# Kernel optimization log

Measured on AMD Instinct MI355X. Metric: run time of the kernel, lower is better.

Reference implementation:

```python
import jax, jax.numpy as jnp
import numpy as np
import math

NUM_CLASSES = 80
MAX_ANCHOR_MATCHES = 10
ALPHA = 0.5
BETA = 6.0
EPSILON = 1e-9        # label-encoder epsilon
KEPS = 1e-7           # keras.backend.epsilon() used inside compute_ciou
B, NB = 16, 64        # batch, padded max GT boxes


def make_anchor_points():
    # YOLOv8 @ 640x640: strides 8/16/32 -> 80^2 + 40^2 + 20^2 = 8400 anchors
    pts = []
    for stride, n in [(8, 80), (16, 40), (32, 20)]:
        xs = (jnp.arange(n, dtype=jnp.float32) + 0.5) * stride
        gy, gx = jnp.meshgrid(xs, xs, indexing='ij')
        pts.append(jnp.stack([gx.reshape(-1), gy.reshape(-1)], axis=-1))
    return jnp.concatenate(pts, axis=0)  # (8400, 2)


def setup_inputs() -> dict:
    key = jax.random.key(0)
    k0, k1, k2, k3, k4, k5 = jax.random.split(key, 6)
    anc_points = make_anchor_points()
    NA = anc_points.shape[0]
    pd_scores = jax.random.uniform(k0, (B, NA, NUM_CLASSES), dtype=jnp.float32)
    # predicted boxes roughly centered on anchors
    wh = jax.random.uniform(k1, (B, NA, 2), minval=8.0, maxval=96.0)
    ctr = anc_points[None] + jax.random.normal(k2, (B, NA, 2)) * 8.0
    pd_bboxes = jnp.concatenate([ctr - wh / 2, ctr + wh / 2], axis=-1)
    # ground-truth boxes (xyxy) inside a 640x640 image
    g_wh = jax.random.uniform(k3, (B, NB, 2), minval=16.0, maxval=200.0)
    g_ctr = jax.random.uniform(k4, (B, NB, 2), minval=40.0, maxval=600.0)
    gt_bboxes = jnp.concatenate([g_ctr - g_wh / 2, g_ctr + g_wh / 2], axis=-1)
    gt_labels = jax.random.randint(k5, (B, NB), 0, NUM_CLASSES).astype(jnp.float32)
    # first 48 of 64 padded slots are real boxes
    mask_gt = jnp.broadcast_to(jnp.arange(NB)[None, :, None] < 48, (B, NB, 1))
    return {
        'pd_scores': pd_scores,
        'pd_bboxes': pd_bboxes,
        'anc_points': anc_points,
        'gt_labels': gt_labels,
        'gt_bboxes': gt_bboxes,
        'mask_gt': mask_gt,
    }


def compute_ciou(b1, b2):
    """CIoU between xyxy boxes b1 (gt) and b2 (pred); broadcasts, returns (...,)."""
    x1a, y1a, x2a, y2a = b1[..., 0], b1[..., 1], b1[..., 2], b1[..., 3]
    x1b, y1b, x2b, y2b = b2[..., 0], b2[..., 1], b2[..., 2], b2[..., 3]
    w1 = x2a - x1a
    h1 = y2a - y1a + KEPS
    w2 = x2b - x1b
    h2 = y2b - y1b + KEPS
    inter = (jnp.maximum(jnp.minimum(x2a, x2b) - jnp.maximum(x1a, x1b), 0.0)
             * jnp.maximum(jnp.minimum(y2a, y2b) - jnp.maximum(y1a, y1b), 0.0))
    union = w1 * h1 + w2 * h2 - inter + KEPS
    iou = inter / union
    cw = jnp.maximum(x2a, x2b) - jnp.minimum(x1a, x1b)
    ch = jnp.maximum(y2a, y2b) - jnp.minimum(y1a, y1b)
    c2 = cw * cw + ch * ch + KEPS
    rho2 = ((x1a + x2a) / 2 - (x1b + x2b) / 2) ** 2 + ((y1a + y2a) / 2 - (y1b + y2b) / 2) ** 2
    v = (4.0 / math.pi ** 2) * (jnp.arctan(w2 / h2) - jnp.arctan(w1 / h1)) ** 2
    alpha = v / (v - iou + (1.0 + KEPS))
    return iou - (rho2 / c2 + v * alpha)


def _encode(pd_scores, pd_bboxes, anc_points, gt_labels, gt_bboxes, mask_gt):
    Bn, NA, NC = pd_scores.shape
    NBn = gt_bboxes.shape[1]
    f32 = pd_scores.dtype
    mask_gt_b = mask_gt.astype(bool)                      # (B, NB, 1)

    # --- select_candidates_in_gts: anchor center inside gt box ---
    lt = gt_bboxes[:, :, None, :2]                        # (B, NB, 1, 2)
    rb = gt_bboxes[:, :, None, 2:]
    anc = anc_points[None, None, :, :]                    # (1, 1, NA, 2)
    deltas = jnp.concatenate([anc - lt, rb - anc], -1)    # (B, NB, NA, 4)
    mask_in_gts = jnp.min(deltas, axis=-1) > EPSILON      # (B, NB, NA)
    valid = mask_in_gts & mask_gt_b                       # (B, NB, NA)

    # --- get_box_metrics ---
    lbl = jnp.maximum(gt_labels.astype(jnp.int32), 0)     # (B, NB)
    sc = jnp.take_along_axis(pd_scores, jnp.broadcast_to(lbl[:, None, :], (Bn, NA, NBn)), axis=-1)
    sc = jnp.transpose(sc, (0, 2, 1))                     # (B, NB, NA)
    sc = jnp.where(gt_labels[:, :, None] >= 0, sc, 0.0)
    bbox_scores = jnp.where(valid, sc, 0.0)
    iou = compute_ciou(gt_bboxes[:, :, None, :], pd_bboxes[:, None, :, :])  # (B, NB, NA)
    iou = jnp.where(iou > 0, iou, 0.0)
    overlaps = jnp.where(valid, iou, 0.0)
    align_metric = jnp.power(bbox_scores, ALPHA) * jnp.power(overlaps, BETA)

    # --- select_topk_candidates ---
    k = MAX_ANCHOR_MATCHES
    _, topk_idxs = jax.lax.top_k(align_metric, k)         # (B, NB, k)
    topk_idxs = jnp.where(jnp.broadcast_to(mask_gt_b, (Bn, NBn, k)), topk_idxs, 0)
    bi = jnp.arange(Bn)[:, None, None]
    gi = jnp.arange(NBn)[None, :, None]
    counts = jnp.zeros((Bn, NBn, NA), f32).at[bi, gi, topk_idxs].add(1.0)
    mask_topk = jnp.where(counts > 1, 0.0, counts)        # drop idx-0 duplicates
    mask_pos = mask_topk * mask_in_gts.astype(f32) * mask_gt_b.astype(f32)

    # --- select_highest_overlaps (tie-break anchors matched to >1 gt) ---
    fg_mask = jnp.sum(mask_pos, axis=-2)                  # (B, NA)
    mask_multi = jnp.broadcast_to((fg_mask > 1)[:, None, :], (Bn, NBn, NA))
    max_idx = jnp.argmax(overlaps, axis=1)                # (B, NA)
    is_max = jnp.transpose(jax.nn.one_hot(max_idx, NBn, dtype=f32), (0, 2, 1))
    mask_pos = jnp.where(mask_multi, is_max, mask_pos)
    fg_mask = jnp.sum(mask_pos, axis=-2)
    target_gt_idx = jnp.argmax(mask_pos, axis=-2)         # (B, NA)

    # --- get_targets ---
    target_labels = jnp.take_along_axis(lbl, target_gt_idx, axis=1)          # (B, NA)
    target_bboxes = jnp.take_along_axis(gt_bboxes, target_gt_idx[..., None], axis=1)  # (B, NA, 4)
    target_scores = jax.nn.one_hot(target_labels, NC, dtype=f32)
    target_scores = jnp.where((fg_mask > 0)[..., None], target_scores, 0.0)

    # --- normalize class targets by alignment metric ---
    align_metric = align_metric * mask_pos
    pos_align = jnp.max(align_metric, axis=-1, keepdims=True)                # (B, NB, 1)
    pos_overlaps = jnp.max(overlaps * mask_pos, axis=-1, keepdims=True)
    norm = jnp.max(align_metric * pos_overlaps / (pos_align + EPSILON), axis=-2)[..., None]
    target_scores = target_scores * norm
    return target_bboxes, target_scores, fg_mask


def reference(pd_scores, pd_bboxes, anc_points, gt_labels, gt_bboxes, mask_gt):
    tb, ts, fg = _encode(pd_scores, pd_bboxes, anc_points, gt_labels, gt_bboxes, mask_gt)
    return (jax.lax.stop_gradient(tb), jax.lax.stop_gradient(ts), jax.lax.stop_gradient(fg))
```

## Files before the change

kernel.cpp:

```cpp
#include <hip/hip_runtime.h>
#include <cstdint>
#include <cstddef>

#define NBg 64
#define NCg 80
#define KTOP 10
#define K16 16

typedef unsigned long long u64k;

__device__ __forceinline__ float ciou_dev(float gx1, float gy1, float gx2, float gy2,
                                          float px1, float py1, float px2, float py2) {
#pragma clang fp contract(off)
  const float keps = 1e-7f;
  float w1 = gx2 - gx1;
  float h1 = (gy2 - gy1) + keps;
  float w2 = px2 - px1;
  float h2 = (py2 - py1) + keps;
  float iw = fminf(gx2, px2) - fmaxf(gx1, px1);
  float ih = fminf(gy2, py2) - fmaxf(gy1, py1);
  float inter = fmaxf(iw, 0.0f) * fmaxf(ih, 0.0f);
  float uni = w1 * h1 + w2 * h2 - inter + keps;
  float iou = inter / uni;
  float cw = fmaxf(gx2, px2) - fminf(gx1, px1);
  float ch = fmaxf(gy2, py2) - fminf(gy1, py1);
  float c2 = cw * cw + ch * ch + keps;
  float dx = (gx1 + gx2) * 0.5f - (px1 + px2) * 0.5f;
  float dy = (gy1 + gy2) * 0.5f - (py1 + py2) * 0.5f;
  float rho2 = dx * dx + dy * dy;
  float q2 = w2 / h2;
  float q1 = w1 / h1;
  float t = (float)atan((double)q2) - (float)atan((double)q1);
  float v = 0.4052847345693511f * (t * t);
  float alpha = v / ((v - iou) + 1.0000001f);
  return iou - (rho2 / c2 + v * alpha);
}

__device__ __forceinline__ float am_dev(float sc, float ov) {
  float f1 = (float)sqrt((double)sc);
  double o = (double)ov;
  double o3 = o * o * o;
  return f1 * (float)(o3 * o3);
}

__device__ __forceinline__ u64k mk_key(float am, int a) {
  return ((u64k)__float_as_uint(am) << 32) | (unsigned)(~a);
}

__device__ __forceinline__ void merge16(u64k (&L)[K16], const u64k (&B)[K16]) {
  u64k C[K16];
#pragma unroll
  for (int i = 0; i < K16; i++) {
    u64k x = L[i], y = B[15 - i];
    C[i] = x > y ? x : y;
  }
#pragma unroll
  for (int s = 8; s > 0; s >>= 1) {
#pragma unroll
    for (int i = 0; i < K16; i++) {
      if ((i & s) == 0) {
        u64k x = C[i], y = C[i | s];
        C[i] = x > y ? x : y;
        C[i | s] = x > y ? y : x;
      }
    }
  }
#pragma unroll
  for (int i = 0; i < K16; i++) L[i] = C[i];
}

__global__ void ka_topk(const float* __restrict__ pd_scores,
                        const float* __restrict__ pd_bboxes,
                        const float* __restrict__ anc,
                        const float* __restrict__ gt_labels,
                        const float* __restrict__ gt_bboxes,
                        const int* __restrict__ mask_gt,
                        int* __restrict__ sel,
                        float* __restrict__ posAlign,
                        float* __restrict__ posOv,
                        int NA) {
  int row = blockIdx.x;
  int tid = threadIdx.x;
  int lane = tid & 63;
  int wid = tid >> 6;
  if (tid == 0) { posAlign[row] = 0.0f; posOv[row] = 0.0f; }
  if (!mask_gt[row]) {
    if (tid < KTOP) sel[row * KTOP + tid] = -1;
    return;
  }
  int b = row >> 6;
  const float* g = gt_bboxes + (size_t)row * 4;
  float gx1 = g[0], gy1 = g[1], gx2 = g[2], gy2 = g[3];
  float gl = gt_labels[row];
  int lbl = gl > 0.0f ? (int)gl : 0;
  bool glpos = (gl >= 0.0f);

  auto rect = [&](float s, int n, int& x0, int& y0, int& w, int& h) {
    int i0 = (int)floorf(gx1 / s - 0.5f) - 1; if (i0 < 0) i0 = 0;
    int i1 = (int)ceilf (gx2 / s - 0.5f) + 1; if (i1 > n - 1) i1 = n - 1;
    int j0 = (int)floorf(gy1 / s - 0.5f) - 1; if (j0 < 0) j0 = 0;
    int j1 = (int)ceilf (gy2 / s - 0.5f) + 1; if (j1 > n - 1) j1 = n - 1;
    x0 = i0; y0 = j0;
    w = i1 - i0 + 1; h = j1 - j0 + 1;
    if (w < 0) w = 0;
    if (h < 0) h = 0;
  };
  int x00, y00, w0, h0, x01, y01, w1, h1, x02, y02, w2, h2;
  rect( 8.0f, 80, x00, y00, w0, h0);
  rect(16.0f, 40, x01, y01, w1, h1);
  rect(32.0f, 20, x02, y02, w2, h2);
  int sz0 = w0 * h0, sz1 = w1 * h1, sz2 = w2 * h2;
  int tot = sz0 + sz1 + sz2;

  u64k k[KTOP];
#pragma unroll
  for (int q = 0; q < KTOP; q++) k[q] = 0;

  auto ins = [&](u64k key) {
    if (key > k[KTOP - 1]) {
      k[KTOP - 1] = key;
#pragma unroll
      for (int q = KTOP - 1; q > 0; q--) {
        if (k[q] > k[q - 1]) { u64k t = k[q]; k[q] = k[q - 1]; k[q - 1] = t; }
      }
    }
  };

  for (int c = tid; c < tot; c += 256) {
    int cc, x0, y0, w, nbase, ngrid; float ss;
    if (c < sz0)              { cc = c;              x0 = x00; y0 = y00; w = w0; nbase = 0;    ngrid = 80; ss =  8.0f; }
    else if (c < sz0 + sz1)   { cc = c - sz0;        x0 = x01; y0 = y01; w = w1; nbase = 6400; ngrid = 40; ss = 16.0f; }
    else                      { cc = c - sz0 - sz1;  x0 = x02; y0 = y02; w = w2; nbase = 8000; ngrid = 20; ss = 32.0f; }
    int iy = y0 + cc / w;
    int ix = x0 + cc % w;
    float ax = ((float)ix + 0.5f) * ss;
    float ay = ((float)iy + 0.5f) * ss;
    float dmin = fminf(fminf(ax - gx1, ay - gy1), fminf(gx2 - ax, gy2 - ay));
    if (dmin > 1e-9f) {
      int a = nbase + iy * ngrid + ix;
      const float4 pb = ((const float4*)pd_bboxes)[(size_t)b * NA + a];
      float ci = ciou_dev(gx1, gy1, gx2, gy2, pb.x, pb.y, pb.z, pb.w);
      float ov = ci > 0.0f ? ci : 0.0f;
      float sc = glpos ? pd_scores[((size_t)b * NA + a) * NCg + lbl] : 0.0f;
      ins(mk_key(am_dev(sc, ov), a));
    }
  }

  u64k L[K16];
#pragma unroll
  for (int q = 0; q < KTOP; q++) L[q] = k[q];
#pragma unroll
  for (int q = KTOP; q < K16; q++) L[q] = 0;

#pragma unroll
  for (int step = 0; step < 6; step++) {
    u64k B[K16];
#pragma unroll
    for (int q = 0; q < K16; q++)
      B[q] = __shfl_xor((unsigned long long)L[q], 1 << step, 64);
    merge16(L, B);
  }

  __shared__ u64k xl[4][K16];
  if (lane < K16) xl[wid][lane] = L[lane];
  __syncthreads();
  if (wid == 2) {
    u64k B[K16];
#pragma unroll
    for (int q = 0; q < K16; q++) B[q] = xl[3][q];
    merge16(L, B);
    if (lane < K16) xl[2][lane] = L[lane];
  }
  if (wid == 0) {
    u64k B[K16];
#pragma unroll
    for (int q = 0; q < K16; q++) B[q] = xl[1][q];
    merge16(L, B);
  }
  __syncthreads();
  if (wid == 0) {
    u64k B[K16];
#pragma unroll
    for (int q = 0; q < K16; q++) B[q] = xl[2][q];
    merge16(L, B);
    if (lane == 0) {
      int npos = 0;
#pragma unroll
      for (int q = 0; q < KTOP; q++) if ((L[q] >> 32) != 0) npos++;
      int cand = 0;
      const float2* anc2 = (const float2*)anc;
      for (int slot = 0; slot < KTOP; slot++) {
        int a;
        if (slot < npos) {
          a = (int)~(unsigned)L[slot];
        } else {
          bool moved = true;
          while (moved) {
            moved = false;
#pragma unroll
            for (int q = 0; q < KTOP; q++)
              if (q < npos && (int)~(unsigned)L[q] == cand) { cand++; moved = true; }
          }
          a = cand++;
        }
        float2 ap = anc2[a];
        float dmin = fminf(fminf(ap.x - gx1, ap.y - gy1),
                           fminf(gx2 - ap.x, gy2 - ap.y));
        sel[row * KTOP + slot] = (dmin > 1e-9f) ? a : -1;
      }
    }
  }
}

__global__ void k3_resolve(const float* __restrict__ pd_scores,
                           const float* __restrict__ pd_bboxes,
                           const float* __restrict__ anc,
                           const float* __restrict__ gt_labels,
                           const float* __restrict__ gt_bboxes,
                           const int* __restrict__ mask_gt,
                           const int* __restrict__ sel,
                           int* __restrict__ tgt,
                           float* __restrict__ amv,
                           float* __restrict__ out_tb,
                           float* __restrict__ out_fg,
                           float* __restrict__ posAlign,
                           float* __restrict__ posOv,
                           int NA) {
  int b = blockIdx.y;
  int tid = threadIdx.x;
  int a0 = blockIdx.x * 256;
  int a = a0 + tid;
  __shared__ float4 sg[NBg];
  __shared__ int svalid[NBg];
  __shared__ int slbl[NBg];
  __shared__ int sglpos[NBg];
  __shared__ unsigned int mlo[256];
  __shared__ unsigned int mhi[256];
  mlo[tid] = 0u; mhi[tid] = 0u;
  if (tid < NBg) {
    int j = tid;
    const float* g = gt_bboxes + ((size_t)b * NBg + j) * 4;
    sg[j] = make_float4(g[0], g[1], g[2], g[3]);
    svalid[j] = mask_gt[b * NBg + j];
    float gl = gt_labels[b * NBg + j];
    slbl[j] = gl > 0.0f ? (int)gl : 0;
    sglpos[j] = (gl >= 0.0f) ? 1 : 0;
  }
  __syncthreads();
  for (int i = tid; i < NBg * KTOP; i += 256) {
    int e = sel[b * NBg * KTOP + i];
    int d = e - a0;
    if (d >= 0 && d < 256) {
      int j = i / KTOP;
      unsigned int bit = 1u << (j & 31);
      if (j < 32) atomicOr(&mlo[d], bit); else atomicOr(&mhi[d], bit);
    }
  }
  __syncthreads();
  if (a >= NA) return;
  unsigned int lo = mlo[tid], hi = mhi[tid];
  int cnt = __popc(lo) + __popc(hi);
  int first = lo ? (__ffs(lo) - 1) : (hi ? 32 + __ffs(hi) - 1 : 0);

  float ax = anc[2 * a], ay = anc[2 * a + 1];
  float px1 = 0.f, py1 = 0.f, px2 = 0.f, py2 = 0.f;
  if (cnt > 0) {
    const float* pb = pd_bboxes + ((size_t)b * NA + a) * 4;
    px1 = pb[0]; py1 = pb[1]; px2 = pb[2]; py2 = pb[3];
  }
  int t = 0;
  float fg = 0.0f;
  float ovt = -1.0f;
  if (cnt == 1) {
    t = first; fg = 1.0f;
  } else if (cnt > 1) {
    unsigned bm_lo = 0u, bm_hi = 0u;
    for (int jj = 0; jj < NBg; jj++) {
      if (svalid[jj]) {
        float4 gq = sg[jj];
        float dmin = fminf(fminf(ax - gq.x, ay - gq.y), fminf(gq.z - ax, gq.w - ay));
        if (dmin > 1e-9f) {
          if (jj < 32) bm_lo |= 1u << jj; else bm_hi |= 1u << (jj - 32);
        }
      }
    }
    float best = 0.0f;
    t = 0;
    unsigned m = bm_lo; int base = 0;
    for (int half = 0; half < 2; half++) {
      while (m) {
        int jj = base + __ffs(m) - 1; m &= m - 1;
        float4 gq = sg[jj];
        float ci = ciou_dev(gq.x, gq.y, gq.z, gq.w, px1, py1, px2, py2);
        float ov = ci > 0.0f ? ci : 0.0f;
        if (ov > best) { best = ov; t = jj; }
      }
      m = bm_hi; base = 32;
    }
    fg = 1.0f;
    ovt = best;
  }
  tgt[(size_t)b * NA + a] = t;
  out_fg[(size_t)b * NA + a] = fg;
  float4 gb = sg[t];
  ((float4*)out_tb)[(size_t)b * NA + a] = gb;
  float amval = 0.0f;
  if (fg > 0.0f) {
    float ov;
    if (ovt >= 0.0f) {
      ov = ovt;
    } else {
      float ci = ciou_dev(gb.x, gb.y, gb.z, gb.w, px1, py1, px2, py2);
      ov = ci > 0.0f ? ci : 0.0f;
    }
    float sc = sglpos[t] ? pd_scores[((size_t)b * NA + a) * NCg + slbl[t]] : 0.0f;
    amval = am_dev(sc, ov);
    atomicMax((int*)(posAlign + b * NBg + t), __float_as_int(amval));
    atomicMax((int*)(posOv + b * NBg + t), __float_as_int(ov));
  }
  amv[(size_t)b * NA + a] = amval;
}

__global__ void k5_scores(const float* __restrict__ gt_labels,
                          const int* __restrict__ tgt,
                          const float* __restrict__ out_fg,
                          const float* __restrict__ amv,
                          const float* __restrict__ posAlign,
                          const float* __restrict__ posOv,
                          float* __restrict__ out_ts,
                          int NA) {
  int b = blockIdx.y;
  int a0 = blockIdx.x * 256;
  int tid = threadIdx.x;
  int a = a0 + tid;
  __shared__ float snorm[256];
  __shared__ int slab[256];
  float norm = 0.0f;
  int lbl = -1;
  if (a < NA) {
    int t = tgt[(size_t)b * NA + a];
    float fg = out_fg[(size_t)b * NA + a];
    if (fg > 0.0f) {
      float av = amv[(size_t)b * NA + a];
      norm = av * posOv[b * NBg + t] / (posAlign[b * NBg + t] + 1e-9f);
      float gl = gt_labels[b * NBg + t];
      lbl = gl > 0.0f ? (int)gl : 0;
    }
  }
  snorm[tid] = norm;
  slab[tid] = lbl;
  __syncthreads();
  int nanch = NA - a0; if (nanch > 256) nanch = 256;
  int nf4 = nanch * (NCg / 4);
  float4* o = (float4*)(out_ts + ((size_t)b * NA + a0) * NCg);
  for (int i = tid; i < nf4; i += 256) {
    int aa = i / (NCg / 4);
    int c0 = (i % (NCg / 4)) * 4;
    int lb = slab[aa];
    float nv = snorm[aa];
    float4 w = make_float4(0.0f, 0.0f, 0.0f, 0.0f);
    int d = lb - c0;
    if (d >= 0 && d < 4) ((float*)&w)[d] = nv;
    o[i] = w;
  }
}

extern "C" void kernel_launch(void* const* d_in, const int* in_sizes, int n_in,
                              void* d_out, int out_size, void* d_ws, size_t ws_size,
                              hipStream_t stream) {
  const float* pd_scores = (const float*)d_in[0];
  const float* pd_bboxes = (const float*)d_in[1];
  const float* anc       = (const float*)d_in[2];
  const float* gt_labels = (const float*)d_in[3];
  const float* gt_bboxes = (const float*)d_in[4];
  const int*   mask_gt   = (const int*)d_in[5];

  int NA = in_sizes[2] / 2;
  int B  = in_sizes[3] / NBg;
  size_t nBA = (size_t)B * NA;

  float* out_tb = (float*)d_out;
  float* out_ts = out_tb + nBA * 4;
  float* out_fg = out_ts + nBA * NCg;

  char* ws = (char*)d_ws;
  size_t off = 0;
  int* sel = (int*)(ws + off);                off += (size_t)B * NBg * KTOP * 4;
  int* tgt = (int*)(ws + off);                off += nBA * 4;
  float* amv = (float*)(ws + off);            off += nBA * 4;
  float* posAlign = (float*)(ws + off);       off += (size_t)B * NBg * 4;
  float* posOv = (float*)(ws + off);          off += (size_t)B * NBg * 4;

  dim3 blk(256);
  int rows = B * NBg;
  ka_topk<<<rows, blk, 0, stream>>>(pd_scores, pd_bboxes, anc, gt_labels,
                                    gt_bboxes, mask_gt, sel, posAlign, posOv, NA);
  dim3 gA((NA + 255) / 256, B);
  k3_resolve<<<gA, blk, 0, stream>>>(pd_scores, pd_bboxes, anc, gt_labels,
                                     gt_bboxes, mask_gt, sel, tgt, amv,
                                     out_tb, out_fg, posAlign, posOv, NA);
  k5_scores<<<gA, blk, 0, stream>>>(gt_labels, tgt, out_fg, amv, posAlign, posOv,
                                    out_ts, NA);
}
```

Measured before the change: 158.4 us.

## Fuse top-k, resolve and score kernels into one persistent kernel with grid barriers

Merges the three kernels into a single launch of 512 blocks that sync through a software grid barrier. Each block handles two GT rows for top-k selection, using 128 threads per row, and then up to two anchor tiles for the resolve and score phases. Per-anchor target and alignment values now stay in shared memory, so the tgt/amv workspace round trips and two kernel launches are removed. It adds a memset launch and depends on every block being co-resident; if they are not, the spin barrier can deadlock.

After: 324.2 us. 2.05x slower.

```diff
diff --git a/kernel.cpp b/kernel.cpp
--- a/kernel.cpp
+++ b/kernel.cpp
@@ -69,88 +69,131 @@
   for (int i = 0; i < K16; i++) L[i] = C[i];
 }
 
-__global__ void ka_topk(const float* __restrict__ pd_scores,
-                        const float* __restrict__ pd_bboxes,
-                        const float* __restrict__ anc,
-                        const float* __restrict__ gt_labels,
-                        const float* __restrict__ gt_bboxes,
-                        const int* __restrict__ mask_gt,
-                        int* __restrict__ sel,
-                        float* __restrict__ posAlign,
-                        float* __restrict__ posOv,
-                        int NA) {
-  int row = blockIdx.x;
+__device__ __forceinline__ void grid_barrier(unsigned* cnt, unsigned* gen) {
+  __syncthreads();
+  if (threadIdx.x == 0) {
+    __threadfence();
+    unsigned g = __hip_atomic_load(gen, __ATOMIC_RELAXED, __HIP_MEMORY_SCOPE_AGENT);
+    unsigned arrived =
+        __hip_atomic_fetch_add(cnt, 1u, __ATOMIC_ACQ_REL, __HIP_MEMORY_SCOPE_AGENT) + 1;
+    if (arrived == gridDim.x) {
+      __hip_atomic_store(cnt, 0u, __ATOMIC_RELAXED, __HIP_MEMORY_SCOPE_AGENT);
+      __hip_atomic_fetch_add(gen, 1u, __ATOMIC_RELEASE, __HIP_MEMORY_SCOPE_AGENT);
+    } else {
+      while (__hip_atomic_load(gen, __ATOMIC_ACQUIRE, __HIP_MEMORY_SCOPE_AGENT) == g) {
+        __builtin_amdgcn_s_sleep(8);
+      }
+    }
+    __threadfence();
+  }
+  __syncthreads();
+}
+
+__global__ __launch_bounds__(256, 2) void fused_all(
+    const float* __restrict__ pd_scores,
+    const float* __restrict__ pd_bboxes,
+    const float* __restrict__ anc,
+    const float* __restrict__ gt_labels,
+    const float* __restrict__ gt_bboxes,
+    const int* __restrict__ mask_gt,
+    int* __restrict__ sel,
+    float* __restrict__ posAlign,
+    float* __restrict__ posOv,
+    unsigned* __restrict__ bar,
+    float* __restrict__ out_tb,
+    float* __restrict__ out_ts,
+    float* __restrict__ out_fg,
+    int NA, int nTiles, int totalTiles) {
+  int bid = blockIdx.x;
   int tid = threadIdx.x;
   int lane = tid & 63;
-  int wid = tid >> 6;
-  if (tid == 0) { posAlign[row] = 0.0f; posOv[row] = 0.0f; }
-  if (!mask_gt[row]) {
-    if (tid < KTOP) sel[row * KTOP + tid] = -1;
-    return;
-  }
-  int b = row >> 6;
+  int wave = tid >> 6;
+  int half = tid >> 7;
+  int htid = tid & 127;
+
+  __shared__ u64k xl[4][K16];
+  __shared__ float4 sg[NBg];
+  __shared__ int svalid[NBg], slbl[NBg], sglpos[NBg];
+  __shared__ unsigned mlo[256], mhi[256];
+  __shared__ float s_amv[2][256];
+  __shared__ int s_tgt[2][256];
+  __shared__ float spa[NBg], spo[NBg];
+  __shared__ int slbl2[NBg];
+  __shared__ float snorm[256];
+  __shared__ int slab[256];
+
+  const float2* anc2 = (const float2*)anc;
+
+  int row = 2 * bid + half;
+  int rb = row >> 6;
+  if (htid == 0) { posAlign[row] = 0.0f; posOv[row] = 0.0f; }
+  bool rowvalid = mask_gt[row] != 0;
+
   const float* g = gt_bboxes + (size_t)row * 4;
   float gx1 = g[0], gy1 = g[1], gx2 = g[2], gy2 = g[3];
-  float gl = gt_labels[row];
-  int lbl = gl > 0.0f ? (int)gl : 0;
-  bool glpos = (gl >= 0.0f);
-
-  auto rect = [&](float s, int n, int& x0, int& y0, int& w, int& h) {
-    int i0 = (int)floorf(gx1 / s - 0.5f) - 1; if (i0 < 0) i0 = 0;
-    int i1 = (int)ceilf (gx2 / s - 0.5f) + 1; if (i1 > n - 1) i1 = n - 1;
-    int j0 = (int)floorf(gy1 / s - 0.5f) - 1; if (j0 < 0) j0 = 0;
-    int j1 = (int)ceilf (gy2 / s - 0.5f) + 1; if (j1 > n - 1) j1 = n - 1;
-    x0 = i0; y0 = j0;
-    w = i1 - i0 + 1; h = j1 - j0 + 1;
-    if (w < 0) w = 0;
-    if (h < 0) h = 0;
-  };
-  int x00, y00, w0, h0, x01, y01, w1, h1, x02, y02, w2, h2;
-  rect( 8.0f, 80, x00, y00, w0, h0);
-  rect(16.0f, 40, x01, y01, w1, h1);
-  rect(32.0f, 20, x02, y02, w2, h2);
-  int sz0 = w0 * h0, sz1 = w1 * h1, sz2 = w2 * h2;
-  int tot = sz0 + sz1 + sz2;
-
-  u64k k[KTOP];
-#pragma unroll
-  for (int q = 0; q < KTOP; q++) k[q] = 0;
-
-  auto ins = [&](u64k key) {
-    if (key > k[KTOP - 1]) {
-      k[KTOP - 1] = key;
-#pragma unroll
-      for (int q = KTOP - 1; q > 0; q--) {
-        if (k[q] > k[q - 1]) { u64k t = k[q]; k[q] = k[q - 1]; k[q - 1] = t; }
-      }
-    }
-  };
-
-  for (int c = tid; c < tot; c += 256) {
-    int cc, x0, y0, w, nbase, ngrid; float ss;
-    if (c < sz0)              { cc = c;              x0 = x00; y0 = y00; w = w0; nbase = 0;    ngrid = 80; ss =  8.0f; }
-    else if (c < sz0 + sz1)   { cc = c - sz0;        x0 = x01; y0 = y01; w = w1; nbase = 6400; ngrid = 40; ss = 16.0f; }
-    else                      { cc = c - sz0 - sz1;  x0 = x02; y0 = y02; w = w2; nbase = 8000; ngrid = 20; ss = 32.0f; }
-    int iy = y0 + cc / w;
-    int ix = x0 + cc % w;
-    float ax = ((float)ix + 0.5f) * ss;
-    float ay = ((float)iy + 0.5f) * ss;
-    float dmin = fminf(fminf(ax - gx1, ay - gy1), fminf(gx2 - ax, gy2 - ay));
-    if (dmin > 1e-9f) {
-      int a = nbase + iy * ngrid + ix;
-      const float4 pb = ((const float4*)pd_bboxes)[(size_t)b * NA + a];
-      float ci = ciou_dev(gx1, gy1, gx2, gy2, pb.x, pb.y, pb.z, pb.w);
-      float ov = ci > 0.0f ? ci : 0.0f;
-      float sc = glpos ? pd_scores[((size_t)b * NA + a) * NCg + lbl] : 0.0f;
-      ins(mk_key(am_dev(sc, ov), a));
-    }
-  }
 
   u64k L[K16];
 #pragma unroll
-  for (int q = 0; q < KTOP; q++) L[q] = k[q];
-#pragma unroll
-  for (int q = KTOP; q < K16; q++) L[q] = 0;
+  for (int q = 0; q < K16; q++) L[q] = 0;
+
+  if (rowvalid) {
+    float gl = gt_labels[row];
+    int lbl = gl > 0.0f ? (int)gl : 0;
+    bool glpos = (gl >= 0.0f);
+
+    auto rect = [&](float s, int n, int& x0, int& y0, int& w, int& h) {
+      int i0 = (int)floorf(gx1 / s - 0.5f) - 1; if (i0 < 0) i0 = 0;
+      int i1 = (int)ceilf (gx2 / s - 0.5f) + 1; if (i1 > n - 1) i1 = n - 1;
+      int j0 = (int)floorf(gy1 / s - 0.5f) - 1; if (j0 < 0) j0 = 0;
+      int j1 = (int)ceilf (gy2 / s - 0.5f) + 1; if (j1 > n - 1) j1 = n - 1;
+      x0 = i0; y0 = j0;
+      w = i1 - i0 + 1; h = j1 - j0 + 1;
+      if (w < 0) w = 0;
+      if (h < 0) h = 0;
+    };
+    int x00, y00, w0, h0, x01, y01, w1, h1, x02, y02, w2, h2;
+    rect( 8.0f, 80, x00, y00, w0, h0);
+    rect(16.0f, 40, x01, y01, w1, h1);
+    rect(32.0f, 20, x02, y02, w2, h2);
+    int sz0 = w0 * h0, sz1 = w1 * h1, sz2 = w2 * h2;
+    int tot = sz0 + sz1 + sz2;
+
+    u64k k[KTOP];
+#pragma unroll
+    for (int q = 0; q < KTOP; q++) k[q] = 0;
+
+    auto ins = [&](u64k key) {
+      if (key > k[KTOP - 1]) {
+        k[KTOP - 1] = key;
+#pragma unroll
+        for (int q = KTOP - 1; q > 0; q--) {
+          if (k[q] > k[q - 1]) { u64k t = k[q]; k[q] = k[q - 1]; k[q - 1] = t; }
+        }
+      }
+    };
+
+    for (int c = htid; c < tot; c += 128) {
+      int cc, x0, y0, w, nbase, ngrid; float ss;
+      if (c < sz0)            { cc = c;             x0 = x00; y0 = y00; w = w0; nbase = 0;    ngrid = 80; ss =  8.0f; }
+      else if (c < sz0 + sz1) { cc = c - sz0;       x0 = x01; y0 = y01; w = w1; nbase = 6400; ngrid = 40; ss = 16.0f; }
+      else                    { cc = c - sz0 - sz1; x0 = x02; y0 = y02; w = w2; nbase = 8000; ngrid = 20; ss = 32.0f; }
+      int iy = y0 + cc / w;
+      int ix = x0 + cc % w;
+      float ax = ((float)ix + 0.5f) * ss;
+      float ay = ((float)iy + 0.5f) * ss;
+      float dmin = fminf(fminf(ax - gx1, ay - gy1), fminf(gx2 - ax, gy2 - ay));
+      if (dmin > 1e-9f) {
+        int a = nbase + iy * ngrid + ix;
+        const float4 pb = ((const float4*)pd_bboxes)[(size_t)rb * NA + a];
+        float ci = ciou_dev(gx1, gy1, gx2, gy2, pb.x, pb.y, pb.z, pb.w);
+        float ov = ci > 0.0f ? ci : 0.0f;
+        float sc = glpos ? pd_scores[((size_t)rb * NA + a) * NCg + lbl] : 0.0f;
+        ins(mk_key(am_dev(sc, ov), a));
+      }
+    }
+#pragma unroll
+    for (int q = 0; q < KTOP; q++) L[q] = k[q];
+  }
 
 #pragma unroll
   for (int step = 0; step < 6; step++) {
@@ -160,35 +203,18 @@
       B[q] = __shfl_xor((unsigned long long)L[q], 1 << step, 64);
     merge16(L, B);
   }
-
-  __shared__ u64k xl[4][K16];
-  if (lane < K16) xl[wid][lane] = L[lane];
+  if (lane < K16) xl[wave][lane] = L[lane];
   __syncthreads();
-  if (wid == 2) {
+  if ((wave & 1) == 0) {
     u64k B[K16];
 #pragma unroll
-    for (int q = 0; q < K16; q++) B[q] = xl[3][q];
+    for (int q = 0; q < K16; q++) B[q] = xl[wave | 1][q];
     merge16(L, B);
-    if (lane < K16) xl[2][lane] = L[lane];
-  }
-  if (wid == 0) {
-    u64k B[K16];
-#pragma unroll
-    for (int q = 0; q < K16; q++) B[q] = xl[1][q];
-    merge16(L, B);
-  }
-  __syncthreads();
-  if (wid == 0) {
-    u64k B[K16];
-#pragma unroll
-    for (int q = 0; q < K16; q++) B[q] = xl[2][q];
-    merge16(L, B);
-    if (lane == 0) {
+    if (lane == 0 && rowvalid) {
       int npos = 0;
 #pragma unroll
       for (int q = 0; q < KTOP; q++) if ((L[q] >> 32) != 0) npos++;
       int cand = 0;
-      const float2* anc2 = (const float2*)anc;
       for (int slot = 0; slot < KTOP; slot++) {
         int a;
         if (slot < npos) {
@@ -210,158 +236,155 @@
       }
     }
   }
-}
-
-__global__ void k3_resolve(const float* __restrict__ pd_scores,
-                           const float* __restrict__ pd_bboxes,
-                           const float* __restrict__ anc,
-                           const float* __restrict__ gt_labels,
-                           const float* __restrict__ gt_bboxes,
-                           const int* __restrict__ mask_gt,
-                           const int* __restrict__ sel,
-                           int* __restrict__ tgt,
-                           float* __restrict__ amv,
-                           float* __restrict__ out_tb,
-                           float* __restrict__ out_fg,
-                           float* __restrict__ posAlign,
-                           float* __restrict__ posOv,
-                           int NA) {
-  int b = blockIdx.y;
-  int tid = threadIdx.x;
-  int a0 = blockIdx.x * 256;
-  int a = a0 + tid;
-  __shared__ float4 sg[NBg];
-  __shared__ int svalid[NBg];
-  __shared__ int slbl[NBg];
-  __shared__ int sglpos[NBg];
-  __shared__ unsigned int mlo[256];
-  __shared__ unsigned int mhi[256];
-  mlo[tid] = 0u; mhi[tid] = 0u;
-  if (tid < NBg) {
-    int j = tid;
-    const float* g = gt_bboxes + ((size_t)b * NBg + j) * 4;
-    sg[j] = make_float4(g[0], g[1], g[2], g[3]);
-    svalid[j] = mask_gt[b * NBg + j];
-    float gl = gt_labels[b * NBg + j];
-    slbl[j] = gl > 0.0f ? (int)gl : 0;
-    sglpos[j] = (gl >= 0.0f) ? 1 : 0;
-  }
-  __syncthreads();
-  for (int i = tid; i < NBg * KTOP; i += 256) {
-    int e = sel[b * NBg * KTOP + i];
-    int d = e - a0;
-    if (d >= 0 && d < 256) {
-      int j = i / KTOP;
-      unsigned int bit = 1u << (j & 31);
-      if (j < 32) atomicOr(&mlo[d], bit); else atomicOr(&mhi[d], bit);
-    }
-  }
-  __syncthreads();
-  if (a >= NA) return;
-  unsigned int lo = mlo[tid], hi = mhi[tid];
-  int cnt = __popc(lo) + __popc(hi);
-  int first = lo ? (__ffs(lo) - 1) : (hi ? 32 + __ffs(hi) - 1 : 0);
-
-  float ax = anc[2 * a], ay = anc[2 * a + 1];
-  float px1 = 0.f, py1 = 0.f, px2 = 0.f, py2 = 0.f;
-  if (cnt > 0) {
-    const float* pb = pd_bboxes + ((size_t)b * NA + a) * 4;
-    px1 = pb[0]; py1 = pb[1]; px2 = pb[2]; py2 = pb[3];
-  }
-  int t = 0;
-  float fg = 0.0f;
-  float ovt = -1.0f;
-  if (cnt == 1) {
-    t = first; fg = 1.0f;
-  } else if (cnt > 1) {
-    unsigned bm_lo = 0u, bm_hi = 0u;
-    for (int jj = 0; jj < NBg; jj++) {
-      if (svalid[jj]) {
-        float4 gq = sg[jj];
-        float dmin = fminf(fminf(ax - gq.x, ay - gq.y), fminf(gq.z - ax, gq.w - ay));
-        if (dmin > 1e-9f) {
-          if (jj < 32) bm_lo |= 1u << jj; else bm_hi |= 1u << (jj - 32);
-        }
-      }
-    }
-    float best = 0.0f;
-    t = 0;
-    unsigned m = bm_lo; int base = 0;
-    for (int half = 0; half < 2; half++) {
-      while (m) {
-        int jj = base + __ffs(m) - 1; m &= m - 1;
-        float4 gq = sg[jj];
-        float ci = ciou_dev(gq.x, gq.y, gq.z, gq.w, px1, py1, px2, py2);
-        float ov = ci > 0.0f ? ci : 0.0f;
-        if (ov > best) { best = ov; t = jj; }
-      }
-      m = bm_hi; base = 32;
-    }
-    fg = 1.0f;
-    ovt = best;
-  }
-  tgt[(size_t)b * NA + a] = t;
-  out_fg[(size_t)b * NA + a] = fg;
-  float4 gb = sg[t];
-  ((float4*)out_tb)[(size_t)b * NA + a] = gb;
-  float amval = 0.0f;
-  if (fg > 0.0f) {
-    float ov;
-    if (ovt >= 0.0f) {
-      ov = ovt;
-    } else {
-      float ci = ciou_dev(gb.x, gb.y, gb.z, gb.w, px1, py1, px2, py2);
-      ov = ci > 0.0f ? ci : 0.0f;
-    }
-    float sc = sglpos[t] ? pd_scores[((size_t)b * NA + a) * NCg + slbl[t]] : 0.0f;
-    amval = am_dev(sc, ov);
-    atomicMax((int*)(posAlign + b * NBg + t), __float_as_int(amval));
-    atomicMax((int*)(posOv + b * NBg + t), __float_as_int(ov));
-  }
-  amv[(size_t)b * NA + a] = amval;
-}
-
-__global__ void k5_scores(const float* __restrict__ gt_labels,
-                          const int* __restrict__ tgt,
-                          const float* __restrict__ out_fg,
-                          const float* __restrict__ amv,
-                          const float* __restrict__ posAlign,
-                          const float* __restrict__ posOv,
-                          float* __restrict__ out_ts,
-                          int NA) {
-  int b = blockIdx.y;
-  int a0 = blockIdx.x * 256;
-  int tid = threadIdx.x;
-  int a = a0 + tid;
-  __shared__ float snorm[256];
-  __shared__ int slab[256];
-  float norm = 0.0f;
-  int lbl = -1;
-  if (a < NA) {
-    int t = tgt[(size_t)b * NA + a];
-    float fg = out_fg[(size_t)b * NA + a];
-    if (fg > 0.0f) {
-      float av = amv[(size_t)b * NA + a];
-      norm = av * posOv[b * NBg + t] / (posAlign[b * NBg + t] + 1e-9f);
-      float gl = gt_labels[b * NBg + t];
-      lbl = gl > 0.0f ? (int)gl : 0;
-    }
-  }
-  snorm[tid] = norm;
-  slab[tid] = lbl;
-  __syncthreads();
-  int nanch = NA - a0; if (nanch > 256) nanch = 256;
-  int nf4 = nanch * (NCg / 4);
-  float4* o = (float4*)(out_ts + ((size_t)b * NA + a0) * NCg);
-  for (int i = tid; i < nf4; i += 256) {
-    int aa = i / (NCg / 4);
-    int c0 = (i % (NCg / 4)) * 4;
-    int lb = slab[aa];
-    float nv = snorm[aa];
-    float4 w = make_float4(0.0f, 0.0f, 0.0f, 0.0f);
-    int d = lb - c0;
-    if (d >= 0 && d < 4) ((float*)&w)[d] = nv;
-    o[i] = w;
+  if (!rowvalid && htid < KTOP) sel[row * KTOP + htid] = -1;
+
+  grid_barrier(&bar[0], &bar[1]);
+
+  int extra = totalTiles - gridDim.x;
+  for (int ti = 0; ti < 2; ti++) {
+    int t = (ti == 0) ? bid : (bid < extra ? (int)gridDim.x + bid : -1);
+    __syncthreads();
+    int b = 0, a0 = 0, a = 0;
+    if (t >= 0) {
+      b = t / nTiles;
+      a0 = (t % nTiles) * 256;
+      a = a0 + tid;
+      mlo[tid] = 0u; mhi[tid] = 0u;
+      if (tid < NBg) {
+        int j = tid;
+        const float* gg = gt_bboxes + ((size_t)b * NBg + j) * 4;
+        sg[j] = make_float4(gg[0], gg[1], gg[2], gg[3]);
+        svalid[j] = mask_gt[b * NBg + j];
+        float gl = gt_labels[b * NBg + j];
+        slbl[j] = gl > 0.0f ? (int)gl : 0;
+        sglpos[j] = (gl >= 0.0f) ? 1 : 0;
+      }
+    }
+    __syncthreads();
+    if (t >= 0) {
+      for (int i = tid; i < NBg * KTOP; i += 256) {
+        int e = sel[b * NBg * KTOP + i];
+        int d = e - a0;
+        if (d >= 0 && d < 256) {
+          int j = i / KTOP;
+          unsigned bit = 1u << (j & 31);
+          if (j < 32) atomicOr(&mlo[d], bit); else atomicOr(&mhi[d], bit);
+        }
+      }
+    }
+    __syncthreads();
+    if (t >= 0 && a < NA) {
+      unsigned lo = mlo[tid], hi = mhi[tid];
+      int cnt = __popc(lo) + __popc(hi);
+      int first = lo ? (__ffs(lo) - 1) : (hi ? 32 + __ffs(hi) - 1 : 0);
+
+      float ax = anc[2 * a], ay = anc[2 * a + 1];
+      float px1 = 0.f, py1 = 0.f, px2 = 0.f, py2 = 0.f;
+      if (cnt > 0) {
+        const float* pb = pd_bboxes + ((size_t)b * NA + a) * 4;
+        px1 = pb[0]; py1 = pb[1]; px2 = pb[2]; py2 = pb[3];
+      }
+      int tt = 0;
+      float fg = 0.0f;
+      float ovt = -1.0f;
+      if (cnt == 1) {
+        tt = first; fg = 1.0f;
+      } else if (cnt > 1) {
+        unsigned bm_lo = 0u, bm_hi = 0u;
+        for (int jj = 0; jj < NBg; jj++) {
+          if (svalid[jj]) {
+            float4 gq = sg[jj];
+            float dmin = fminf(fminf(ax - gq.x, ay - gq.y), fminf(gq.z - ax, gq.w - ay));
+            if (dmin > 1e-9f) {
+              if (jj < 32) bm_lo |= 1u << jj; else bm_hi |= 1u << (jj - 32);
+            }
+          }
+        }
+        float best = 0.0f;
+        tt = 0;
+        unsigned m = bm_lo; int base = 0;
+        for (int hh = 0; hh < 2; hh++) {
+          while (m) {
+            int jj = base + __ffs(m) - 1; m &= m - 1;
+            float4 gq = sg[jj];
+            float ci = ciou_dev(gq.x, gq.y, gq.z, gq.w, px1, py1, px2, py2);
+            float ov = ci > 0.0f ? ci : 0.0f;
+            if (ov > best) { best = ov; tt = jj; }
+          }
+          m = bm_hi; base = 32;
+        }
+        fg = 1.0f;
+        ovt = best;
+      }
+      out_fg[(size_t)b * NA + a] = fg;
+      float4 gb = sg[tt];
+      ((float4*)out_tb)[(size_t)b * NA + a] = gb;
+      float amval = 0.0f;
+      if (fg > 0.0f) {
+        float ov;
+        if (ovt >= 0.0f) {
+          ov = ovt;
+        } else {
+          float ci = ciou_dev(gb.x, gb.y, gb.z, gb.w, px1, py1, px2, py2);
+          ov = ci > 0.0f ? ci : 0.0f;
+        }
+        float sc = sglpos[tt] ? pd_scores[((size_t)b * NA + a) * NCg + slbl[tt]] : 0.0f;
+        amval = am_dev(sc, ov);
+        atomicMax((int*)(posAlign + b * NBg + tt), __float_as_int(amval));
+        atomicMax((int*)(posOv + b * NBg + tt), __float_as_int(ov));
+      }
+      s_tgt[ti][tid] = (fg > 0.0f) ? tt : -1;
+      s_amv[ti][tid] = amval;
+    }
+  }
+
+  grid_barrier(&bar[0], &bar[1]);
+
+  for (int ti = 0; ti < 2; ti++) {
+    int t = (ti == 0) ? bid : (bid < extra ? (int)gridDim.x + bid : -1);
+    __syncthreads();
+    int b = 0, a0 = 0;
+    if (t >= 0) {
+      b = t / nTiles;
+      a0 = (t % nTiles) * 256;
+      if (tid < NBg) {
+        int idx = b * NBg + tid;
+        spa[tid] = __int_as_float(
+            __hip_atomic_load((int*)&posAlign[idx], __ATOMIC_RELAXED, __HIP_MEMORY_SCOPE_AGENT));
+        spo[tid] = __int_as_float(
+            __hip_atomic_load((int*)&posOv[idx], __ATOMIC_RELAXED, __HIP_MEMORY_SCOPE_AGENT));
+        float gl = gt_labels[idx];
+        slbl2[tid] = gl > 0.0f ? (int)gl : 0;
+      }
+    }
+    __syncthreads();
+    if (t >= 0) {
+      int tt = s_tgt[ti][tid];
+      float norm = 0.0f;
+      int lbl = -1;
+      if (tt >= 0) {
+        norm = s_amv[ti][tid] * spo[tt] / (spa[tt] + 1e-9f);
+        lbl = slbl2[tt];
+      }
+      snorm[tid] = norm;
+      slab[tid] = lbl;
+    }
+    __syncthreads();
+    if (t >= 0) {
+      int nanch = NA - a0; if (nanch > 256) nanch = 256;
+      int nf4 = nanch * (NCg / 4);
+      float4* o = (float4*)(out_ts + ((size_t)b * NA + a0) * NCg);
+      for (int i = tid; i < nf4; i += 256) {
+        int aa = i / (NCg / 4);
+        int c0 = (i % (NCg / 4)) * 4;
+        int lb = slab[aa];
+        float nv = snorm[aa];
+        float4 w = make_float4(0.0f, 0.0f, 0.0f, 0.0f);
+        int d = lb - c0;
+        if (d >= 0 && d < 4) ((float*)&w)[d] = nv;
+        o[i] = w;
+      }
+    }
   }
 }
 
@@ -385,20 +408,18 @@
 
   char* ws = (char*)d_ws;
   size_t off = 0;
+  unsigned* bar = (unsigned*)(ws + off);      off += 256;
   int* sel = (int*)(ws + off);                off += (size_t)B * NBg * KTOP * 4;
-  int* tgt = (int*)(ws + off);                off += nBA * 4;
-  float* amv = (float*)(ws + off);            off += nBA * 4;
   float* posAlign = (float*)(ws + off);       off += (size_t)B * NBg * 4;
   float* posOv = (float*)(ws + off);          off += (size_t)B * NBg * 4;
 
-  dim3 blk(256);
-  int rows = B * NBg;
-  ka_topk<<<rows, blk, 0, stream>>>(pd_scores, pd_bboxes, anc, gt_labels,
-                                    gt_bboxes, mask_gt, sel, posAlign, posOv, NA);
-  dim3 gA((NA + 255) / 256, B);
-  k3_resolve<<<gA, blk, 0, stream>>>(pd_scores, pd_bboxes, anc, gt_labels,
-                                     gt_bboxes, mask_gt, sel, tgt, amv,
-                                     out_tb, out_fg, posAlign, posOv, NA);
-  k5_scores<<<gA, blk, 0, stream>>>(gt_labels, tgt, out_fg, amv, posAlign, posOv,
-                                    out_ts, NA);
-}
+  hipMemsetAsync(bar, 0, 8, stream);
+
+  int nTiles = (NA + 255) / 256;
+  int totalTiles = B * nTiles;
+  int grid = (B * NBg) / 2;
+  fused_all<<<grid, 256, 0, stream>>>(pd_scores, pd_bboxes, anc, gt_labels,
+                                      gt_bboxes, mask_gt, sel, posAlign, posOv,
+                                      bar, out_tb, out_ts, out_fg,
+                                      NA, nTiles, totalTiles);
+}
```
